# Kernel tuning notes

Hardware: AMD Instinct MI355X
Metric: run time of the kernel (lower is better)

## Reference

```python
import jax, jax.numpy as jnp
import numpy as np


def setup_inputs() -> dict:
    key = jax.random.key(0)
    k1, k2 = jax.random.split(key)
    B, N, M = 16, 4096, 4096
    x1 = jax.random.normal(k1, (B, N, 3), dtype=jnp.float32)
    x2 = jax.random.normal(k2, (B, M, 3), dtype=jnp.float32)
    return {"x1": x1, "x2": x2}


def reference(x1, x2) -> jnp.ndarray:
    # x1: [B, N, 3], x2: [B, M, 3]
    # dist_matrix[b, i, j] = ||x1[b,i] - x2[b,j]||^2 via |a|^2 + |b|^2 - 2 a.b
    x1_norm = jnp.sum(x1 * x1, axis=2, keepdims=True)           # [B, N, 1]
    x2_norm = jnp.sum(x2 * x2, axis=2)[:, None, :]              # [B, 1, M]
    cross = jnp.einsum('bnd,bmd->bnm', x1, x2)                  # [B, N, M]
    dist_matrix = x1_norm + x2_norm - 2.0 * cross               # [B, N, M]
    min_1_to_2 = jnp.min(dist_matrix, axis=2)                   # [B, N]
    min_2_to_1 = jnp.min(dist_matrix, axis=1)                   # [B, M]
    chamfer = jnp.mean(min_1_to_2, axis=1) + jnp.mean(min_2_to_1, axis=1)  # [B]
    return chamfer
```

## Files before the change

kernel.cpp:

```cpp
#include <hip/hip_runtime.h>


typedef __attribute__((ext_vector_type(8))) __bf16 bf16x8;
typedef __attribute__((ext_vector_type(16))) float f32x16;

#define PTS 4096
#define TILES 128
#define NB 16

__device__ __forceinline__ unsigned f2bf(float f) {
  unsigned u = __float_as_uint(f);
  return (u + 0x7FFFu + ((u >> 16) & 1u)) >> 16;
}
__device__ __forceinline__ float bf2f(unsigned s) {
  return __uint_as_float(s << 16);
}
__device__ __forceinline__ unsigned pk(unsigned lo, unsigned hi) {
  return (lo & 0xFFFFu) | (hi << 16);
}

__global__ __launch_bounds__(256) void prepack_b(const float* __restrict__ x1,
                                                 const float* __restrict__ x2,
                                                 uint4* __restrict__ Bfr) {
  const int id = blockIdx.x * 256 + threadIdx.x;
  const int d = id >> 16;
  const int b = (id >> 12) & (NB - 1);
  const int j = id & (PTS - 1);
  const float* q = (d ? x1 : x2) + (size_t)(b * PTS + j) * 3;
  const float x = q[0], y = q[1], z = q[2];
  const float sx = -2.f * x, sy = -2.f * y, sz = -2.f * z;
  const unsigned Hx = f2bf(sx), Hy = f2bf(sy), Hz = f2bf(sz);
  const unsigned Lx = f2bf(sx - bf2f(Hx));
  const unsigned Ly = f2bf(sy - bf2f(Hy));
  const unsigned Lz = f2bf(sz - bf2f(Hz));
  const float n = fmaf(x, x, fmaf(y, y, z * z));
  const unsigned nh = f2bf(n), nl = f2bf(n - bf2f(nh));
  const unsigned one = 0x3F80u;
  uint4 w0, w1;
  w0.x = pk(Hx, Hy); w0.y = pk(Hz, Lx); w0.z = pk(Ly, Lz); w0.w = pk(Hx, Hy);
  w1.x = pk(Hz, nh); w1.y = pk(nl, one); w1.z = pk(one, 0u); w1.w = 0u;
  uint4* base =
      Bfr + ((size_t)((d * NB + b) * TILES + (j >> 5)) * 2) * 32 + (j & 31);
  base[0]  = w0;
  base[32] = w1;
}

__global__ __launch_bounds__(128, 3) void chamfer_main(
    const float* __restrict__ x1, const float* __restrict__ x2,
    const uint4* __restrict__ Bfr, unsigned* __restrict__ rowm) {
  const int rb = blockIdx.x;
  const int b  = blockIdx.y;
  const int z  = blockIdx.z;
  const int d  = z >> 1, ch = z & 1;

  const int tid  = threadIdx.x;
  const int lane = tid & 63;
  const int half = lane >> 5;
  const int l31  = lane & 31;
  const int wave = tid >> 6;

  const float* P = d ? x2 : x1;
  const int t0 = rb * 4 + wave * 2;
  bf16x8 af[2];
#pragma unroll
  for (int rr = 0; rr < 2; ++rr) {
    const int r = (t0 + rr) * 32 + l31;
    const float* p = P + (size_t)(b * PTS + r) * 3;
    const float x = p[0], y = p[1], zc = p[2];
    const unsigned hx = f2bf(x), hy = f2bf(y), hz = f2bf(zc);
    const unsigned lx = f2bf(x - bf2f(hx));
    const unsigned ly = f2bf(y - bf2f(hy));
    const unsigned lz = f2bf(zc - bf2f(hz));
    const float n = fmaf(x, x, fmaf(y, y, zc * zc));
    const unsigned nh = f2bf(n), nl = f2bf(n - bf2f(nh));
    const unsigned one = 0x3F80u;
    uint4 w0, w1;
    w0.x = pk(hx, hy); w0.y = pk(hz, hx); w0.z = pk(hy, hz); w0.w = pk(lx, ly);
    w1.x = pk(lz, one); w1.y = pk(one, nh); w1.z = pk(nl, 0u); w1.w = 0u;
    uint4 w;
    w.x = half ? w1.x : w0.x; w.y = half ? w1.y : w0.y;
    w.z = half ? w1.z : w0.z; w.w = half ? w1.w : w0.w;
    af[rr] = *(const bf16x8*)&w;
  }
  const bf16x8 af0 = af[0], af1 = af[1];

  f32x16 zero;
#pragma unroll
  for (int e = 0; e < 16; ++e) zero[e] = 0.f;

  float rm0[16], rm1[16];
#pragma unroll
  for (int e = 0; e < 16; ++e) { rm0[e] = 3.0e38f; rm1[e] = 3.0e38f; }

  const uint4* bp =
      Bfr + ((size_t)((d * NB + b) * TILES + ch * 64) * 2) * 32;
  const int off = half * 32 + l31;
  bf16x8 b0 = *(const bf16x8*)&bp[off];
  bf16x8 b1 = *(const bf16x8*)&bp[64 + off];
#pragma unroll 2
  for (int jt = 0; jt < 64; jt += 2) {
    const int nx = (jt + 2) & 63;
    const bf16x8 n0 = *(const bf16x8*)&bp[nx * 64 + off];
    const bf16x8 n1 = *(const bf16x8*)&bp[(nx + 1) * 64 + off];
    const f32x16 a00 =
        __builtin_amdgcn_mfma_f32_32x32x16_bf16(af0, b0, zero, 0, 0, 0);
    const f32x16 a01 =
        __builtin_amdgcn_mfma_f32_32x32x16_bf16(af0, b1, zero, 0, 0, 0);
#pragma unroll
    for (int e = 0; e < 16; ++e)
      rm0[e] = fminf(fminf(a00[e], a01[e]), rm0[e]);
    const f32x16 a10 =
        __builtin_amdgcn_mfma_f32_32x32x16_bf16(af1, b0, zero, 0, 0, 0);
    const f32x16 a11 =
        __builtin_amdgcn_mfma_f32_32x32x16_bf16(af1, b1, zero, 0, 0, 0);
#pragma unroll
    for (int e = 0; e < 16; ++e)
      rm1[e] = fminf(fminf(a10[e], a11[e]), rm1[e]);
    b0 = n0; b1 = n1;
  }

  unsigned* rbase = rowm + (size_t)(d * NB + b) * PTS + rb * 128 + wave * 64;
#pragma unroll
  for (int e = 0; e < 16; ++e) {
    float v = rm0[e];
    v = fminf(v, __shfl_xor(v, 1));
    v = fminf(v, __shfl_xor(v, 2));
    v = fminf(v, __shfl_xor(v, 4));
    v = fminf(v, __shfl_xor(v, 8));
    v = fminf(v, __shfl_xor(v, 16));
    if (l31 == e) {
      const int rl = (e & 3) + 8 * (e >> 2) + 4 * half;
      atomicMin(rbase + rl, __float_as_uint(fmaxf(v, 0.f)));
    }
  }
#pragma unroll
  for (int e = 0; e < 16; ++e) {
    float v = rm1[e];
    v = fminf(v, __shfl_xor(v, 1));
    v = fminf(v, __shfl_xor(v, 2));
    v = fminf(v, __shfl_xor(v, 4));
    v = fminf(v, __shfl_xor(v, 8));
    v = fminf(v, __shfl_xor(v, 16));
    if (l31 == e) {
      const int rl = 32 + (e & 3) + 8 * (e >> 2) + 4 * half;
      atomicMin(rbase + rl, __float_as_uint(fmaxf(v, 0.f)));
    }
  }
}

__global__ __launch_bounds__(256) void reduce_rows(
    const unsigned* __restrict__ rowm, float* __restrict__ out) {
  const int b = blockIdx.x;
  const int tid = threadIdx.x;
  const unsigned* r0 = rowm + (size_t)b * PTS;
  const unsigned* r1 = rowm + (size_t)(NB + b) * PTS;
  float s = 0.f;
  for (int i = tid; i < PTS; i += 256)
    s += __uint_as_float(r0[i]) + __uint_as_float(r1[i]);
  s += __shfl_xor(s, 1);
  s += __shfl_xor(s, 2);
  s += __shfl_xor(s, 4);
  s += __shfl_xor(s, 8);
  s += __shfl_xor(s, 16);
  s += __shfl_xor(s, 32);
  __shared__ float acc[4];
  if ((tid & 63) == 0) acc[tid >> 6] = s;
  __syncthreads();
  if (tid == 0) out[b] = (acc[0] + acc[1] + acc[2] + acc[3]) * (1.f / PTS);
}

extern "C" void kernel_launch(void* const* d_in, const int* in_sizes, int n_in,
                              void* d_out, int out_size, void* d_ws,
                              size_t ws_size, hipStream_t stream) {
  const float* x1 = (const float*)d_in[0];
  const float* x2 = (const float*)d_in[1];
  float* out = (float*)d_out;

  uint4* Bfr = (uint4*)d_ws;
  unsigned* rowm = (unsigned*)((char*)d_ws + (size_t)2 * NB * TILES * 2 * 32 * 16);
  hipMemsetAsync(rowm, 0xFF, (size_t)2 * NB * PTS * 4, stream);

  prepack_b<<<(2 * NB * PTS) / 256, 256, 0, stream>>>(x1, x2, Bfr);
  dim3 grid(PTS / 128, NB, 4);
  chamfer_main<<<grid, 128, 0, stream>>>(x1, x2, Bfr, rowm);
  reduce_rows<<<NB, 256, 0, stream>>>(rowm, out);
}
```

Measured before the change: 92.62 us.

## Fold rowmin init into prepack, use 256-thread blocks, deepen B-fragment prefetch

The separate memset of the row-min buffer is removed; prepack_b now writes +inf into rowm, which saves one launch and one pass over memory. chamfer_main moves from 128-thread to 256-thread blocks on a new 2D grid whose flattened x index interleaves direction, batch and column half. Each wave now prefetches B fragments four tiles ahead through a double buffer instead of one pair ahead. The deeper buffer raises register use, and the launch-bounds change to (256,4) could cause spills or lower occupancy.

```diff
diff --git a/kernel.cpp b/kernel.cpp
--- a/kernel.cpp
+++ b/kernel.cpp
@@ -21,8 +21,10 @@
 
 __global__ __launch_bounds__(256) void prepack_b(const float* __restrict__ x1,
                                                  const float* __restrict__ x2,
-                                                 uint4* __restrict__ Bfr) {
+                                                 uint4* __restrict__ Bfr,
+                                                 unsigned* __restrict__ rowm) {
   const int id = blockIdx.x * 256 + threadIdx.x;
+  rowm[id] = 0x7F800000u;
   const int d = id >> 16;
   const int b = (id >> 12) & (NB - 1);
   const int j = id & (PTS - 1);
@@ -45,13 +47,14 @@
   base[32] = w1;
 }
 
-__global__ __launch_bounds__(128, 3) void chamfer_main(
+__global__ __launch_bounds__(256, 4) void chamfer_main(
     const float* __restrict__ x1, const float* __restrict__ x2,
     const uint4* __restrict__ Bfr, unsigned* __restrict__ rowm) {
-  const int rb = blockIdx.x;
-  const int b  = blockIdx.y;
-  const int z  = blockIdx.z;
-  const int d  = z >> 1, ch = z & 1;
+  const int s  = blockIdx.x;
+  const int d  = s & 1;
+  const int b  = (s >> 1) & (NB - 1);
+  const int ch = (s >> 5) & 1;
+  const int rg = blockIdx.y;
 
   const int tid  = threadIdx.x;
   const int lane = tid & 63;
@@ -60,7 +63,7 @@
   const int wave = tid >> 6;
 
   const float* P = d ? x2 : x1;
-  const int t0 = rb * 4 + wave * 2;
+  const int t0 = rg * 8 + wave * 2;
   bf16x8 af[2];
 #pragma unroll
   for (int rr = 0; rr < 2; ++rr) {
@@ -92,34 +95,41 @@
 #pragma unroll
   for (int e = 0; e < 16; ++e) { rm0[e] = 3.0e38f; rm1[e] = 3.0e38f; }
 
-  const uint4* bp =
-      Bfr + ((size_t)((d * NB + b) * TILES + ch * 64) * 2) * 32;
+  const uint4* bp = Bfr + ((size_t)((d * NB + b) * TILES + ch * 64) * 2) * 32;
   const int off = half * 32 + l31;
-  bf16x8 b0 = *(const bf16x8*)&bp[off];
-  bf16x8 b1 = *(const bf16x8*)&bp[64 + off];
+  bf16x8 buf[8];
+#pragma unroll
+  for (int t = 0; t < 4; ++t) buf[t] = *(const bf16x8*)&bp[t * 64 + off];
+
 #pragma unroll 2
-  for (int jt = 0; jt < 64; jt += 2) {
-    const int nx = (jt + 2) & 63;
-    const bf16x8 n0 = *(const bf16x8*)&bp[nx * 64 + off];
-    const bf16x8 n1 = *(const bf16x8*)&bp[(nx + 1) * 64 + off];
-    const f32x16 a00 =
-        __builtin_amdgcn_mfma_f32_32x32x16_bf16(af0, b0, zero, 0, 0, 0);
-    const f32x16 a01 =
-        __builtin_amdgcn_mfma_f32_32x32x16_bf16(af0, b1, zero, 0, 0, 0);
+  for (int g = 0; g < 16; ++g) {
+    const int cur = (g & 1) * 4;
+    const int nxt = ((g + 1) & 1) * 4;
+    const int pf  = ((g + 1) & 15) * 4;
 #pragma unroll
-    for (int e = 0; e < 16; ++e)
-      rm0[e] = fminf(fminf(a00[e], a01[e]), rm0[e]);
-    const f32x16 a10 =
-        __builtin_amdgcn_mfma_f32_32x32x16_bf16(af1, b0, zero, 0, 0, 0);
-    const f32x16 a11 =
-        __builtin_amdgcn_mfma_f32_32x32x16_bf16(af1, b1, zero, 0, 0, 0);
+    for (int t = 0; t < 4; ++t)
+      buf[nxt + t] = *(const bf16x8*)&bp[(pf + t) * 64 + off];
 #pragma unroll
-    for (int e = 0; e < 16; ++e)
-      rm1[e] = fminf(fminf(a10[e], a11[e]), rm1[e]);
-    b0 = n0; b1 = n1;
+    for (int t = 0; t < 4; t += 2) {
+      const bf16x8 b0 = buf[cur + t], b1 = buf[cur + t + 1];
+      const f32x16 a00 =
+          __builtin_amdgcn_mfma_f32_32x32x16_bf16(af0, b0, zero, 0, 0, 0);
+      const f32x16 a01 =
+          __builtin_amdgcn_mfma_f32_32x32x16_bf16(af0, b1, zero, 0, 0, 0);
+#pragma unroll
+      for (int e = 0; e < 16; ++e)
+        rm0[e] = fminf(fminf(a00[e], a01[e]), rm0[e]);
+      const f32x16 a10 =
+          __builtin_amdgcn_mfma_f32_32x32x16_bf16(af1, b0, zero, 0, 0, 0);
+      const f32x16 a11 =
+          __builtin_amdgcn_mfma_f32_32x32x16_bf16(af1, b1, zero, 0, 0, 0);
+#pragma unroll
+      for (int e = 0; e < 16; ++e)
+        rm1[e] = fminf(fminf(a10[e], a11[e]), rm1[e]);
+    }
   }
 
-  unsigned* rbase = rowm + (size_t)(d * NB + b) * PTS + rb * 128 + wave * 64;
+  unsigned* rbase = rowm + (size_t)(d * NB + b) * PTS + t0 * 32;
 #pragma unroll
   for (int e = 0; e < 16; ++e) {
     float v = rm0[e];
@@ -177,11 +187,11 @@
   float* out = (float*)d_out;
 
   uint4* Bfr = (uint4*)d_ws;
-  unsigned* rowm = (unsigned*)((char*)d_ws + (size_t)2 * NB * TILES * 2 * 32 * 16);
-  hipMemsetAsync(rowm, 0xFF, (size_t)2 * NB * PTS * 4, stream);
+  unsigned* rowm =
+      (unsigned*)((char*)d_ws + (size_t)2 * NB * TILES * 2 * 32 * 16);
 
-  prepack_b<<<(2 * NB * PTS) / 256, 256, 0, stream>>>(x1, x2, Bfr);
-  dim3 grid(PTS / 128, NB, 4);
-  chamfer_main<<<grid, 128, 0, stream>>>(x1, x2, Bfr, rowm);
+  prepack_b<<<(2 * NB * PTS) / 256, 256, 0, stream>>>(x1, x2, Bfr, rowm);
+  dim3 grid(64, NB);
+  chamfer_main<<<grid, 256, 0, stream>>>(x1, x2, Bfr, rowm);
   reduce_rows<<<NB, 256, 0, stream>>>(rowm, out);
 }
```

New measurement: 88.19 us. 1.05x faster.
